# Optimization experiments

Hardware: AMD Instinct MI355X
Metric: run time of the kernel (lower is better)

Reference implementation:

```python
import jax, jax.numpy as jnp
import numpy as np

NUM_NODES = 50000
NUM_EDGES = 800000
NUM_GRAPHS = 64
EMBED = 128
HIDDEN = 128
LAYERS = 3
CLUSTERS = 16
OUT_DIM = 128
MAX_DEG = 64
EPS = 1e-5


def setup_inputs() -> dict:
    key = jax.random.key(0)
    ks = jax.random.split(key, 16)
    deg_idx = jax.random.randint(ks[0], (NUM_NODES,), 0, MAX_DEG + 1)
    edge_index = jax.random.randint(ks[1], (2, NUM_EDGES), 0, NUM_NODES)
    batch = jnp.sort(jax.random.randint(ks[2], (NUM_NODES,), 0, NUM_GRAPHS))
    s = 0.05
    emb = jax.random.normal(ks[3], (MAX_DEG + 1, EMBED), jnp.float32) * s
    Wl = jax.random.normal(ks[4], (LAYERS, HIDDEN, HIDDEN), jnp.float32) * s
    bl = jnp.zeros((LAYERS, HIDDEN), jnp.float32)
    Wr = jax.random.normal(ks[5], (LAYERS, HIDDEN, HIDDEN), jnp.float32) * s
    gamma = jnp.ones((LAYERS, HIDDEN), jnp.float32)
    beta = jnp.zeros((LAYERS, HIDDEN), jnp.float32)
    attn_W = jax.random.normal(ks[6], (HIDDEN, CLUSTERS), jnp.float32) * s
    attn_b = jnp.zeros((CLUSTERS,), jnp.float32)
    out_W = jax.random.normal(ks[7], (HIDDEN, OUT_DIM), jnp.float32) * s
    out_b = jnp.zeros((OUT_DIM,), jnp.float32)
    return {"emb": emb, "Wl": Wl, "bl": bl, "Wr": Wr, "gamma": gamma,
            "beta": beta, "attn_W": attn_W, "attn_b": attn_b,
            "out_W": out_W, "out_b": out_b, "deg_idx": deg_idx,
            "edge_index": edge_index, "batch": batch}


def reference(emb, Wl, bl, Wr, gamma, beta, attn_W, attn_b, out_W, out_b,
              deg_idx, edge_index, batch):
    N = deg_idx.shape[0]
    src, dst = edge_index[0], edge_index[1]
    x = emb[deg_idx]  # [N, EMBED]
    for l in range(Wl.shape[0]):
        # SAGEConv (mean aggr): lin_l(mean_j x_j) + lin_r(x); lin_r has no bias
        msg_sum = jax.ops.segment_sum(x[src], dst, num_segments=N)
        cnt = jax.ops.segment_sum(jnp.ones((src.shape[0], 1), x.dtype), dst,
                                  num_segments=N)
        mean = msg_sum / jnp.maximum(cnt, 1.0)
        x = mean @ Wl[l] + bl[l] + x @ Wr[l]
        # BatchNorm1d (training-mode batch stats, biased variance)
        mu = x.mean(axis=0)
        var = jnp.mean((x - mu) ** 2, axis=0)
        x = (x - mu) * jax.lax.rsqrt(var + EPS) * gamma[l] + beta[l]
        x = jax.nn.relu(x)  # dropout is identity in eval
    scores = x @ attn_W + attn_b  # [N, C] (num_heads == 1 -> squeeze)
    # per-graph softmax over nodes (segment softmax along dim 0)
    smax = jax.ops.segment_max(scores, batch, num_segments=NUM_GRAPHS)
    e = jnp.exp(scores - smax[batch])
    denom = jax.ops.segment_sum(e, batch, num_segments=NUM_GRAPHS)
    w = e / denom[batch]  # [N, C]
    # c_b = w_b^T @ x_b  -> segment-weighted sums: [B, C, H]
    clust = jax.ops.segment_sum(w[:, :, None] * x[:, None, :], batch,
                                num_segments=NUM_GRAPHS)
    return clust @ out_W + out_b  # [B, C, OUT_DIM]
```

## Files before the change

kernel.cpp:

```cpp
#include <hip/hip_runtime.h>

typedef unsigned short u16;
typedef unsigned int   u32;

#define H    128
#define C    16
#define ODIM 128

typedef short bf16x8 __attribute__((ext_vector_type(8)));
typedef float f32x4  __attribute__((ext_vector_type(4)));
typedef float f32x2v __attribute__((ext_vector_type(2)));

#define WSP 272
#define NP  256

__device__ __forceinline__ float bf2f(u32 v){
  union { u32 i; float f; } t; t.i = v << 16; return t.f;
}
__device__ __forceinline__ u16 f2bf(float f){
  u32 u = __float_as_uint(f);
  u32 r = u + 0x7fffu + ((u >> 16) & 1u);
  return (u16)(r >> 16);
}
__device__ __forceinline__ u32 pack2(float a, float b){
  return (u32)f2bf(a) | ((u32)f2bf(b) << 16);
}
__device__ __forceinline__ u32 pack_fp8x4(float a, float b, float c, float d){
  int p = __builtin_amdgcn_cvt_pk_fp8_f32(a, b, 0, false);
  p     = __builtin_amdgcn_cvt_pk_fp8_f32(c, d, p, true);
  return (u32)p;
}

__global__ __launch_bounds__(256) void k_setup(const float* __restrict__ emb,
    const int* __restrict__ deg, u16* __restrict__ xb, u32* __restrict__ xq,
    const int* __restrict__ batch, int* __restrict__ gs,
    const float* __restrict__ Wl, const float* __restrict__ Wr,
    u16* __restrict__ Wt, const int* __restrict__ ei,
    int* __restrict__ blkhist, int N, int B, int NB, int E, int chunk,
    int g0, int g1, int g2){
  __shared__ __align__(16) char smem[4608];
  int bid = blockIdx.x, tid = threadIdx.x;
  if (bid < g0){
    int i = bid*256 + tid;
    if (i < N*32){
      int n = i >> 5, q = i & 31;
      int d = deg[n];
      float4 v = ((const float4*)(emb + (size_t)d*H))[q];
      uint2 o; o.x = pack2(v.x, v.y); o.y = pack2(v.z, v.w);
      ((uint2*)(xb + (size_t)n*H))[q] = o;
      xq[i] = pack_fp8x4(v.x, v.y, v.z, v.w);
    }
  } else if (bid < g1){
    int n = (bid - g0)*256 + tid;
    if (n < N){
      int b = batch[n];
      if (n == 0){ for (int g = 0; g <= b; g++) gs[g] = 0; }
      else {
        int pb = batch[n-1];
        for (int g = pb+1; g <= b; g++) gs[g] = n;
      }
      if (n == N-1){ for (int g = b+1; g <= B; g++) gs[g] = N; }
    }
  } else if (bid < g2){
    u16 (*T)[18] = (u16(*)[18])smem;
    int b = bid - g1;
    int strip = b & 7, half = (b >> 3) & 1, l = b >> 4;
    const float* M = (half ? Wr : Wl) + (size_t)l*H*H;
    int k0 = strip * 16;
    #pragma unroll
    for (int j = 0; j < 8; j++){
      int u = tid + j*256;
      int kk = u >> 7, h = u & 127;
      T[h][kk] = f2bf(M[(size_t)(k0 + kk)*H + h]);
    }
    __syncthreads();
    #pragma unroll
    for (int j = 0; j < 8; j++){
      int u = tid + j*256;
      int h = u >> 4, k16 = u & 15;
      Wt[((size_t)(l*H + h))*256 + half*128 + k0 + k16] = T[h][k16];
    }
  } else {
    int* hist = (int*)smem;
    int blk = bid - g2;
    for (int b = tid; b < NB; b += 256) hist[b] = 0;
    __syncthreads();
    int start = blk*chunk, end = min(E, start + chunk);
    for (int e = start + tid; e < end; e += 256)
      atomicAdd(&hist[ei[E + e] >> 7], 1);
    __syncthreads();
    for (int b = tid; b < NB; b += 256) blkhist[b*NP + blk] = hist[b];
  }
}

__global__ __launch_bounds__(256) void k_scanA(const int* __restrict__ in,
    int* __restrict__ out, int* __restrict__ bsum, int n){
  __shared__ int wsum[4];
  int tid = threadIdx.x;
  int base = blockIdx.x*1024 + tid*4;
  int v0 = (base+0 < n) ? in[base+0] : 0;
  int v1 = (base+1 < n) ? in[base+1] : 0;
  int v2 = (base+2 < n) ? in[base+2] : 0;
  int v3 = (base+3 < n) ? in[base+3] : 0;
  int tsum = v0+v1+v2+v3;
  int lane = tid & 63, w = tid >> 6;
  int incl = tsum;
  for (int d = 1; d < 64; d <<= 1){
    int t = __shfl_up(incl, d, 64);
    if (lane >= d) incl += t;
  }
  if (lane == 63) wsum[w] = incl;
  __syncthreads();
  int woff = 0;
  for (int i = 0; i < w; i++) woff += wsum[i];
  int excl = woff + incl - tsum;
  if (base+0 < n) out[base+0] = excl;
  if (base+1 < n) out[base+1] = excl + v0;
  if (base+2 < n) out[base+2] = excl + v0 + v1;
  if (base+3 < n) out[base+3] = excl + v0 + v1 + v2;
  if (tid == 255) bsum[blockIdx.x] = woff + incl;
}

__global__ __launch_bounds__(256) void k_scanB(const int* __restrict__ bsum,
    int* __restrict__ boff, int nb){
  __shared__ int ws[4];
  int tid = threadIdx.x;
  int v = (tid < nb) ? bsum[tid] : 0;
  int lane = tid & 63, w = tid >> 6;
  int incl = v;
  for (int d = 1; d < 64; d <<= 1){
    int t = __shfl_up(incl, d, 64);
    if (lane >= d) incl += t;
  }
  if (lane == 63) ws[w] = incl;
  __syncthreads();
  int woff = 0;
  for (int i = 0; i < w; i++) woff += ws[i];
  boff[tid] = woff + incl - v;
}

__global__ __launch_bounds__(256) void k_place(const int* __restrict__ ei,
    const int* __restrict__ bases, const int* __restrict__ boff,
    int2* __restrict__ pairs, int NB, int E, int chunk){
  __shared__ int cursor[400];
  int blk = blockIdx.x, tid = threadIdx.x;
  for (int b = tid; b < NB; b += 256){
    int i = b*NP + blk;
    cursor[b] = bases[i] + boff[i >> 10];
  }
  __syncthreads();
  int start = blk*chunk, end = min(E, start + chunk);
  for (int e = start + tid; e < end; e += 256){
    int s = ei[e], d = ei[E + e];
    int pos = atomicAdd(&cursor[d >> 7], 1);
    pairs[pos] = make_int2(s, d);
  }
}

__global__ __launch_bounds__(256) void k_cnt_place(const int2* __restrict__ pairs,
    const int* __restrict__ bases, const int* __restrict__ boff,
    int* __restrict__ rowptr, int* __restrict__ col, int NB, int N, int E){
  int b = blockIdx.x, tid = threadIdx.x;
  int i0 = b*NP;
  int bstart = bases[i0] + boff[i0 >> 10];
  int bend = E;
  if (b+1 < NB){ int i1 = (b+1)*NP; bend = bases[i1] + boff[i1 >> 10]; }
  __shared__ int cnt[128], sc[128], rank[128];
  if (tid < 128) cnt[tid] = 0;
  __syncthreads();
  for (int e = bstart + tid; e < bend; e += 256)
    atomicAdd(&cnt[pairs[e].y & 127], 1);
  __syncthreads();
  if (tid < 128) sc[tid] = cnt[tid];
  for (int d = 1; d < 128; d <<= 1){
    int v = 0;
    __syncthreads();
    if (tid < 128 && tid >= d) v = sc[tid - d];
    __syncthreads();
    if (tid < 128) sc[tid] += v;
  }
  __syncthreads();
  if (tid < 128){
    int excl = sc[tid] - cnt[tid];
    rank[tid] = bstart + excl;
    int node = b*128 + tid;
    if (node < N) rowptr[node] = bstart + excl;
  }
  if (b == NB-1 && tid == 0) rowptr[N] = E;
  __syncthreads();
  for (int e = bstart + tid; e < bend; e += 256){
    int2 p = pairs[e];
    int pos = atomicAdd(&rank[p.y & 127], 1);
    col[pos] = p.x;
  }
}

__device__ __forceinline__ void dec16v(f32x2v* a, uint4 v){
  a[0] += __builtin_amdgcn_cvt_pk_f32_fp8((int)v.x, false);
  a[1] += __builtin_amdgcn_cvt_pk_f32_fp8((int)v.x, true );
  a[2] += __builtin_amdgcn_cvt_pk_f32_fp8((int)v.y, false);
  a[3] += __builtin_amdgcn_cvt_pk_f32_fp8((int)v.y, true );
  a[4] += __builtin_amdgcn_cvt_pk_f32_fp8((int)v.z, false);
  a[5] += __builtin_amdgcn_cvt_pk_f32_fp8((int)v.z, true );
  a[6] += __builtin_amdgcn_cvt_pk_f32_fp8((int)v.w, false);
  a[7] += __builtin_amdgcn_cvt_pk_f32_fp8((int)v.w, true );
}

__global__ __launch_bounds__(256) void k_agg(const u32* __restrict__ xq,
    const int* __restrict__ rowptr, const int* __restrict__ col,
    u16* __restrict__ meanb, int N){
  int wid  = (blockIdx.x*256 + threadIdx.x) >> 6;
  int lane = threadIdx.x & 63;
  if (wid >= N) return;
  int r0 = rowptr[wid], r1 = rowptr[wid+1];
  int grp = lane >> 3, fl = lane & 7;
  const u32* xf = xq + fl*4;
  f32x2v a[8];
  #pragma unroll
  for (int j = 0; j < 8; j++) a[j] = (f32x2v){0.f, 0.f};
  int e = r0 + grp;
  for (; e + 8 < r1; e += 16){
    uint4 v = *(const uint4*)(xf + (size_t)col[e]*32);
    uint4 u = *(const uint4*)(xf + (size_t)col[e+8]*32);
    dec16v(a, v);
    dec16v(a, u);
  }
  if (e < r1){
    uint4 v = *(const uint4*)(xf + (size_t)col[e]*32);
    dec16v(a, v);
  }
  #pragma unroll
  for (int j = 0; j < 8; j++){
    a[j].x += __shfl_xor(a[j].x, 8, 64);  a[j].y += __shfl_xor(a[j].y, 8, 64);
    a[j].x += __shfl_xor(a[j].x, 16, 64); a[j].y += __shfl_xor(a[j].y, 16, 64);
    a[j].x += __shfl_xor(a[j].x, 32, 64); a[j].y += __shfl_xor(a[j].y, 32, 64);
  }
  if (grp == 0){
    float invc = 1.0f / (float)max(r1 - r0, 1);
    uint4 o0, o1;
    o0.x = pack2(a[0].x*invc, a[0].y*invc);
    o0.y = pack2(a[1].x*invc, a[1].y*invc);
    o0.z = pack2(a[2].x*invc, a[2].y*invc);
    o0.w = pack2(a[3].x*invc, a[3].y*invc);
    o1.x = pack2(a[4].x*invc, a[4].y*invc);
    o1.y = pack2(a[5].x*invc, a[5].y*invc);
    o1.z = pack2(a[6].x*invc, a[6].y*invc);
    o1.w = pack2(a[7].x*invc, a[7].y*invc);
    u16* mp = meanb + (size_t)wid*H + fl*16;
    *(uint4*)mp       = o0;
    *(uint4*)(mp + 8) = o1;
  }
}

__global__ __launch_bounds__(256) void k_linear(const u16* __restrict__ meanb,
    const u16* __restrict__ xb, const u16* __restrict__ Wt,
    const float* __restrict__ bl, u16* __restrict__ x2b,
    float* __restrict__ pstats, int N){
  __shared__ u16 Ws[128][WSP];
  __shared__ float Sh[128], Qh[128];
  int tid = threadIdx.x;
  if (tid < 128){ Sh[tid] = 0.f; Qh[tid] = 0.f; }
  int lane = tid & 63, w = tid >> 6;
  int mlane = lane & 15, quad = lane >> 4;
  int node = blockIdx.x*64 + w*16 + mlane;
  const u16* arow_m = meanb + (size_t)node*H + quad*8;
  const u16* arow_x = xb   + (size_t)node*H + quad*8;
  bf16x8 af[8];
  #pragma unroll
  for (int kk = 0; kk < 4; kk++){
    af[kk]     = *(const bf16x8*)(arow_m + kk*32);
    af[kk + 4] = *(const bf16x8*)(arow_x + kk*32);
  }
  #pragma unroll
  for (int j = 0; j < 16; j++){
    int u = tid + j*256;
    int row = u >> 5, seg = u & 31;
    uint4 v = ((const uint4*)(Wt + (size_t)row*256))[seg];
    *(uint4*)&Ws[row][seg*8] = v;
  }
  __syncthreads();
  f32x4 acc[8];
  #pragma unroll
  for (int t = 0; t < 8; t++) acc[t] = (f32x4){0.f, 0.f, 0.f, 0.f};
  #pragma unroll
  for (int kk = 0; kk < 8; kk++){
    #pragma unroll
    for (int t = 0; t < 8; t++){
      bf16x8 b = *(const bf16x8*)&Ws[t*16 + mlane][kk*32 + quad*8];
      acc[t] = __builtin_amdgcn_mfma_f32_16x16x32_bf16(af[kk], b, acc[t], 0, 0, 0);
    }
  }
  #pragma unroll
  for (int t = 0; t < 8; t++){
    int h = t*16 + mlane;
    float bv = bl[h];
    float s = 0.f, q = 0.f;
    #pragma unroll
    for (int r = 0; r < 4; r++){
      int nd = blockIdx.x*64 + w*16 + quad*4 + r;
      if (nd < N){
        float v = acc[t][r] + bv;
        x2b[(size_t)nd*H + h] = f2bf(v);
        s += v; q = fmaf(v, v, q);
      }
    }
    s += __shfl_xor(s, 16, 64); s += __shfl_xor(s, 32, 64);
    q += __shfl_xor(q, 16, 64); q += __shfl_xor(q, 32, 64);
    if (quad == 0){
      atomicAdd(&Sh[h], s);
      atomicAdd(&Qh[h], q);
    }
  }
  __syncthreads();
  {
    float v = (tid < 128) ? Sh[tid] : Qh[tid - 128];
    pstats[(size_t)blockIdx.x*256 + tid] = v;
  }
}

__global__ __launch_bounds__(256) void k_statred(const float* __restrict__ pstats,
    float* __restrict__ stats, int nblk){
  __shared__ float red[4];
  int c = blockIdx.x, tid = threadIdx.x;
  float s = 0.f;
  for (int b = tid; b < nblk; b += 256)
    s += pstats[(size_t)b*256 + c];
  s += __shfl_xor(s, 1, 64);  s += __shfl_xor(s, 2, 64);
  s += __shfl_xor(s, 4, 64);  s += __shfl_xor(s, 8, 64);
  s += __shfl_xor(s, 16, 64); s += __shfl_xor(s, 32, 64);
  if ((tid & 63) == 0) red[tid >> 6] = s;
  __syncthreads();
  if (tid == 0) stats[c] = red[0] + red[1] + red[2] + red[3];
}

__global__ __launch_bounds__(256) void k_bnrelu(const u16* __restrict__ x2b,
    const float* __restrict__ stats, const float* __restrict__ gamma,
    const float* __restrict__ beta, u16* __restrict__ xb, u32* __restrict__ xq,
    int N, float invN,
    const float* __restrict__ attn_W, const float* __restrict__ attn_b,
    float* __restrict__ escore, int do_scores){
  __shared__ float xs[8][132];
  __shared__ float aw[H*C];
  __shared__ float ab[C];
  int tid = threadIdx.x;
  int i = blockIdx.x*256 + tid;
  bool active = (i < N*32);
  int h = (tid & 31) * 4;
  float r[4] = {0.f, 0.f, 0.f, 0.f};
  if (active){
    uint2 o2 = ((const uint2*)x2b)[i];
    float vv[4] = {bf2f(o2.x & 0xffff), bf2f(o2.x >> 16),
                   bf2f(o2.y & 0xffff), bf2f(o2.y >> 16)};
    #pragma unroll
    for (int j = 0; j < 4; j++){
      float mu  = stats[h+j] * invN;
      float var = fmaf(-mu, mu, stats[H + h + j] * invN);
      float sc  = rsqrtf(var + 1e-5f) * gamma[h+j];
      float bi  = beta[h+j];
      r[j] = fmaxf(fmaf(vv[j] - mu, sc, bi), 0.0f);
    }
    uint2 o; o.x = pack2(r[0], r[1]); o.y = pack2(r[2], r[3]);
    ((uint2*)xb)[i] = o;
    xq[i] = pack_fp8x4(r[0], r[1], r[2], r[3]);
  }
  if (do_scores){
    #pragma unroll
    for (int j = 0; j < 8; j++) aw[tid + j*256] = attn_W[tid + j*256];
    if (tid < C) ab[tid] = attn_b[tid];
    int ln = tid >> 5;
    if (active){
      xs[ln][h+0]=r[0]; xs[ln][h+1]=r[1]; xs[ln][h+2]=r[2]; xs[ln][h+3]=r[3];
    }
    __syncthreads();
    if (tid < 128){
      int n2 = tid >> 4, c = tid & 15;
      int node = blockIdx.x*8 + n2;
      if (node < N){
        float acc = ab[c];
        #pragma unroll 4
        for (int k = 0; k < H; k++)
          acc = fmaf(xs[n2][k], aw[k*C + c], acc);
        escore[(size_t)node*C + c] = __expf(acc);
      }
    }
  }
}

__global__ __launch_bounds__(256) void k_clust(const u16* __restrict__ xb,
    const float* __restrict__ escore, const int* __restrict__ gs,
    float* __restrict__ partial){
  int g = blockIdx.x >> 4, b = blockIdx.x & 15;
  int h = threadIdx.x & 127, cg = threadIdx.x >> 7;
  int a = gs[g], e2 = gs[g+1];
  float acc[8] = {0,0,0,0,0,0,0,0};
  for (int n = a + b; n < e2; n += 16){
    float xv = bf2f(xb[(size_t)n*H + h]);
    const float4* ep = (const float4*)(escore + (size_t)n*C) + cg*2;
    float4 e0 = ep[0], e1 = ep[1];
    acc[0] = fmaf(e0.x, xv, acc[0]);
    acc[1] = fmaf(e0.y, xv, acc[1]);
    acc[2] = fmaf(e0.z, xv, acc[2]);
    acc[3] = fmaf(e0.w, xv, acc[3]);
    acc[4] = fmaf(e1.x, xv, acc[4]);
    acc[5] = fmaf(e1.y, xv, acc[5]);
    acc[6] = fmaf(e1.z, xv, acc[6]);
    acc[7] = fmaf(e1.w, xv, acc[7]);
  }
  int c0 = cg*8;
  float* dst = partial + (((size_t)(g*16 + b))*C)*H + h;
  #pragma unroll
  for (int r = 0; r < 8; r++)
    dst[(size_t)(c0 + r)*H] = acc[r];
}

__global__ __launch_bounds__(256) void k_out(const float* __restrict__ partial,
    const float* __restrict__ escore, const int* __restrict__ gs,
    const float* __restrict__ out_W, const float* __restrict__ out_b,
    float* __restrict__ out){
  __shared__ float cs[2][128];
  __shared__ float dsum[4];
  int tid = threadIdx.x;
  int r = tid >> 7, h = tid & 127;
  int row = blockIdx.x*2 + r;
  int g = row >> 4, c = row & 15;
  int a = gs[g], b2 = gs[g+1];
  float s = 0.f;
  for (int n = a + h; n < b2; n += 128) s += escore[(size_t)n*C + c];
  s += __shfl_xor(s, 1, 64);  s += __shfl_xor(s, 2, 64);
  s += __shfl_xor(s, 4, 64);  s += __shfl_xor(s, 8, 64);
  s += __shfl_xor(s, 16, 64); s += __shfl_xor(s, 32, 64);
  if ((tid & 63) == 0) dsum[tid >> 6] = s;
  float p = 0.f;
  for (int b = 0; b < 16; b++)
    p += partial[(((size_t)(g*16 + b))*C + c)*H + h];
  cs[r][h] = p;
  __syncthreads();
  float gden = dsum[r*2] + dsum[r*2 + 1];
  float inv = gden > 0.f ? 1.0f / gden : 0.f;
  float acc = 0.f;
  for (int hh = 0; hh < H; hh++)
    acc = fmaf(cs[r][hh], out_W[hh*ODIM + h], acc);
  out[(size_t)row*ODIM + h] = fmaf(acc, inv, out_b[h]);
}

extern "C" void kernel_launch(void* const* d_in, const int* in_sizes, int n_in,
                              void* d_out, int out_size, void* d_ws, size_t ws_size,
                              hipStream_t stream){
  const float* emb    = (const float*)d_in[0];
  const float* Wl     = (const float*)d_in[1];
  const float* bl     = (const float*)d_in[2];
  const float* Wr     = (const float*)d_in[3];
  const float* gamma  = (const float*)d_in[4];
  const float* beta   = (const float*)d_in[5];
  const float* attn_W = (const float*)d_in[6];
  const float* attn_b = (const float*)d_in[7];
  const float* out_W  = (const float*)d_in[8];
  const float* out_b  = (const float*)d_in[9];
  const int* deg    = (const int*)d_in[10];
  const int* ei     = (const int*)d_in[11];
  const int* batch  = (const int*)d_in[12];
  float* out = (float*)d_out;

  const int N = in_sizes[10];
  const int E = in_sizes[11] / 2;
  const int L = in_sizes[1] / (H*H);
  const int B = out_size / (C*ODIM);
  const int NB = (N + 127) >> 7;
  const int nbh = NB * NP;
  const int chunk = (E + NP - 1) / NP;
  const int nblkL = (N + 63) / 64;

  size_t off = 0;
  auto alloc = [&](size_t bytes) -> void* {
    void* p = (char*)d_ws + off;
    off += (bytes + 255) & ~(size_t)255;
    return p;
  };
  u16*   xb     = (u16*)  alloc((size_t)N*H*2);
  u32*   xq     = (u32*)  alloc((size_t)N*H);
  u16*   meanb  = (u16*)  alloc((size_t)N*H*2);
  u16*   x2b    = (u16*)  alloc((size_t)N*H*2);
  int2*  pairs  = (int2*) alloc((size_t)E*8);
  float* partial= (float*)alloc((size_t)B*16*C*H*4);
  u16*   Wt     = (u16*)  alloc((size_t)L*H*256*2);
  float* escore = (float*)alloc((size_t)N*C*4);
  int*   col    = (int*)  alloc((size_t)E*4);
  int*   rowptr = (int*)  alloc((size_t)(N+1)*4);
  int*   blkhist= (int*)  alloc((size_t)nbh*4);
  int*   bases  = (int*)  alloc((size_t)nbh*4);
  int*   bsum   = (int*)  alloc(256*4);
  int*   boff   = (int*)  alloc(256*4);
  int*   gs     = (int*)  alloc((size_t)(B+1)*4);
  float* stats  = (float*)alloc((size_t)L*2*H*4);
  float* pstats = (float*)alloc((size_t)nblkL*256*4);

  int g0 = (N*32 + 255)/256;
  int g1 = g0 + (N + 255)/256;
  int g2 = g1 + L*16;
  int gT = g2 + NP;
  hipLaunchKernelGGL(k_setup, dim3(gT), dim3(256), 0, stream,
                     emb, deg, xb, xq, batch, gs, Wl, Wr, Wt, ei, blkhist,
                     N, B, NB, E, chunk, g0, g1, g2);
  int nblkS = (nbh + 1023) / 1024;
  hipLaunchKernelGGL(k_scanA, dim3(nblkS), dim3(256), 0, stream, blkhist, bases, bsum, nbh);
  hipLaunchKernelGGL(k_scanB, dim3(1),     dim3(256), 0, stream, bsum, boff, nblkS);
  hipLaunchKernelGGL(k_place, dim3(NP), dim3(256), 0, stream,
                     ei, bases, boff, pairs, NB, E, chunk);
  hipLaunchKernelGGL(k_cnt_place, dim3(NB), dim3(256), 0, stream,
                     pairs, bases, boff, rowptr, col, NB, N, E);

  float invN = 1.0f / (float)N;
  for (int l = 0; l < L; l++){
    hipLaunchKernelGGL(k_agg,    dim3((N+3)/4),  dim3(256), 0, stream, xq, rowptr, col, meanb, N);
    hipLaunchKernelGGL(k_linear, dim3(nblkL),    dim3(256), 0, stream,
                       meanb, xb, Wt + (size_t)l*H*256, bl + (size_t)l*H, x2b,
                       pstats, N);
    hipLaunchKernelGGL(k_statred,dim3(256),      dim3(256), 0, stream, pstats, stats + l*2*H, nblkL);
    hipLaunchKernelGGL(k_bnrelu, dim3((N*32+255)/256), dim3(256), 0, stream,
                       x2b, stats + l*2*H, gamma + (size_t)l*H, beta + (size_t)l*H,
                       xb, xq, N, invN, attn_W, attn_b, escore, (l == L-1) ? 1 : 0);
  }
  hipLaunchKernelGGL(k_clust, dim3(B*16),  dim3(256), 0, stream, xb, escore, gs, partial);
  hipLaunchKernelGGL(k_out,   dim3(B*C/2), dim3(256), 0, stream,
                     partial, escore, gs, out_W, out_b, out);
}
```

Before: 335.5 us.

## Remove scanB and statred launches via inline scan and sharded atomic stats

The single-block bsum scan is now recomputed inside each block of k_place and k_cnt_place, so the separate k_scanB launch goes away. The per-block BatchNorm partial stats are now accumulated with float atomics into 16 shards that are zeroed in k_setup, and each k_bnrelu block sums those shards itself, which drops the k_statred launch every layer. This cuts four kernel launches and their serial gaps. In exchange it adds redundant scan work per block, atomic contention on the shards, and run-to-run nondeterminism in the stats sums.

```diff
diff --git a/kernel.cpp b/kernel.cpp
--- a/kernel.cpp
+++ b/kernel.cpp
@@ -13,6 +13,7 @@
 
 #define WSP 272
 #define NP  256
+#define NSH 16
 
 __device__ __forceinline__ float bf2f(u32 v){
   union { u32 i; float f; } t; t.i = v << 16; return t.f;
@@ -36,12 +37,15 @@
     const int* __restrict__ batch, int* __restrict__ gs,
     const float* __restrict__ Wl, const float* __restrict__ Wr,
     u16* __restrict__ Wt, const int* __restrict__ ei,
-    int* __restrict__ blkhist, int N, int B, int NB, int E, int chunk,
-    int g0, int g1, int g2){
+    int* __restrict__ blkhist, float* __restrict__ statsh,
+    int N, int B, int NB, int E, int chunk,
+    int gz, int g0, int g1, int g2){
   __shared__ __align__(16) char smem[4608];
   int bid = blockIdx.x, tid = threadIdx.x;
-  if (bid < g0){
-    int i = bid*256 + tid;
+  if (bid < gz){
+    statsh[bid*256 + tid] = 0.f;
+  } else if (bid < g0){
+    int i = (bid - gz)*256 + tid;
     if (i < N*32){
       int n = i >> 5, q = i & 31;
       int d = deg[n];
@@ -121,10 +125,9 @@
   if (tid == 255) bsum[blockIdx.x] = woff + incl;
 }
 
-__global__ __launch_bounds__(256) void k_scanB(const int* __restrict__ bsum,
-    int* __restrict__ boff, int nb){
-  __shared__ int ws[4];
-  int tid = threadIdx.x;
+__device__ __forceinline__ void scan_bsum(const int* __restrict__ bsum,
+    int* bo, int nb, int tid){
+  __shared__ int ws2[4];
   int v = (tid < nb) ? bsum[tid] : 0;
   int lane = tid & 63, w = tid >> 6;
   int incl = v;
@@ -132,21 +135,24 @@
     int t = __shfl_up(incl, d, 64);
     if (lane >= d) incl += t;
   }
-  if (lane == 63) ws[w] = incl;
+  if (lane == 63) ws2[w] = incl;
   __syncthreads();
   int woff = 0;
-  for (int i = 0; i < w; i++) woff += ws[i];
-  boff[tid] = woff + incl - v;
+  for (int i = 0; i < w; i++) woff += ws2[i];
+  bo[tid] = woff + incl - v;
+  __syncthreads();
 }
 
 __global__ __launch_bounds__(256) void k_place(const int* __restrict__ ei,
-    const int* __restrict__ bases, const int* __restrict__ boff,
-    int2* __restrict__ pairs, int NB, int E, int chunk){
+    const int* __restrict__ bases, const int* __restrict__ bsum,
+    int2* __restrict__ pairs, int NB, int E, int chunk, int nbs){
   __shared__ int cursor[400];
+  __shared__ int bo[256];
   int blk = blockIdx.x, tid = threadIdx.x;
+  scan_bsum(bsum, bo, nbs, tid);
   for (int b = tid; b < NB; b += 256){
     int i = b*NP + blk;
-    cursor[b] = bases[i] + boff[i >> 10];
+    cursor[b] = bases[i] + bo[i >> 10];
   }
   __syncthreads();
   int start = blk*chunk, end = min(E, start + chunk);
@@ -158,13 +164,16 @@
 }
 
 __global__ __launch_bounds__(256) void k_cnt_place(const int2* __restrict__ pairs,
-    const int* __restrict__ bases, const int* __restrict__ boff,
-    int* __restrict__ rowptr, int* __restrict__ col, int NB, int N, int E){
+    const int* __restrict__ bases, const int* __restrict__ bsum,
+    int* __restrict__ rowptr, int* __restrict__ col,
+    int NB, int N, int E, int nbs){
   int b = blockIdx.x, tid = threadIdx.x;
+  __shared__ int bo[256];
+  scan_bsum(bsum, bo, nbs, tid);
   int i0 = b*NP;
-  int bstart = bases[i0] + boff[i0 >> 10];
+  int bstart = bases[i0] + bo[i0 >> 10];
   int bend = E;
-  if (b+1 < NB){ int i1 = (b+1)*NP; bend = bases[i1] + boff[i1 >> 10]; }
+  if (b+1 < NB){ int i1 = (b+1)*NP; bend = bases[i1] + bo[i1 >> 10]; }
   __shared__ int cnt[128], sc[128], rank[128];
   if (tid < 128) cnt[tid] = 0;
   __syncthreads();
@@ -255,7 +264,7 @@
 __global__ __launch_bounds__(256) void k_linear(const u16* __restrict__ meanb,
     const u16* __restrict__ xb, const u16* __restrict__ Wt,
     const float* __restrict__ bl, u16* __restrict__ x2b,
-    float* __restrict__ pstats, int N){
+    float* __restrict__ statsh_l, int N){
   __shared__ u16 Ws[128][WSP];
   __shared__ float Sh[128], Qh[128];
   int tid = threadIdx.x;
@@ -314,35 +323,28 @@
   __syncthreads();
   {
     float v = (tid < 128) ? Sh[tid] : Qh[tid - 128];
-    pstats[(size_t)blockIdx.x*256 + tid] = v;
-  }
-}
-
-__global__ __launch_bounds__(256) void k_statred(const float* __restrict__ pstats,
-    float* __restrict__ stats, int nblk){
-  __shared__ float red[4];
-  int c = blockIdx.x, tid = threadIdx.x;
-  float s = 0.f;
-  for (int b = tid; b < nblk; b += 256)
-    s += pstats[(size_t)b*256 + c];
-  s += __shfl_xor(s, 1, 64);  s += __shfl_xor(s, 2, 64);
-  s += __shfl_xor(s, 4, 64);  s += __shfl_xor(s, 8, 64);
-  s += __shfl_xor(s, 16, 64); s += __shfl_xor(s, 32, 64);
-  if ((tid & 63) == 0) red[tid >> 6] = s;
-  __syncthreads();
-  if (tid == 0) stats[c] = red[0] + red[1] + red[2] + red[3];
+    atomicAdd(&statsh_l[(blockIdx.x & (NSH-1))*256 + tid], v);
+  }
 }
 
 __global__ __launch_bounds__(256) void k_bnrelu(const u16* __restrict__ x2b,
-    const float* __restrict__ stats, const float* __restrict__ gamma,
+    const float* __restrict__ statsh_l, const float* __restrict__ gamma,
     const float* __restrict__ beta, u16* __restrict__ xb, u32* __restrict__ xq,
     int N, float invN,
     const float* __restrict__ attn_W, const float* __restrict__ attn_b,
     float* __restrict__ escore, int do_scores){
+  __shared__ float st[256];
   __shared__ float xs[8][132];
   __shared__ float aw[H*C];
   __shared__ float ab[C];
   int tid = threadIdx.x;
+  {
+    float sacc = 0.f;
+    #pragma unroll
+    for (int s2 = 0; s2 < NSH; s2++) sacc += statsh_l[s2*256 + tid];
+    st[tid] = sacc;
+  }
+  __syncthreads();
   int i = blockIdx.x*256 + tid;
   bool active = (i < N*32);
   int h = (tid & 31) * 4;
@@ -353,8 +355,8 @@
                    bf2f(o2.y & 0xffff), bf2f(o2.y >> 16)};
     #pragma unroll
     for (int j = 0; j < 4; j++){
-      float mu  = stats[h+j] * invN;
-      float var = fmaf(-mu, mu, stats[H + h + j] * invN);
+      float mu  = st[h+j] * invN;
+      float var = fmaf(-mu, mu, st[H + h + j] * invN);
       float sc  = rsqrtf(var + 1e-5f) * gamma[h+j];
       float bi  = beta[h+j];
       r[j] = fmaxf(fmaf(vv[j] - mu, sc, bi), 0.0f);
@@ -489,35 +491,33 @@
   int*   blkhist= (int*)  alloc((size_t)nbh*4);
   int*   bases  = (int*)  alloc((size_t)nbh*4);
   int*   bsum   = (int*)  alloc(256*4);
-  int*   boff   = (int*)  alloc(256*4);
   int*   gs     = (int*)  alloc((size_t)(B+1)*4);
-  float* stats  = (float*)alloc((size_t)L*2*H*4);
-  float* pstats = (float*)alloc((size_t)nblkL*256*4);
-
-  int g0 = (N*32 + 255)/256;
+  float* statsh = (float*)alloc((size_t)L*NSH*256*4);
+
+  int gz = L*NSH;
+  int g0 = gz + (N*32 + 255)/256;
   int g1 = g0 + (N + 255)/256;
   int g2 = g1 + L*16;
   int gT = g2 + NP;
   hipLaunchKernelGGL(k_setup, dim3(gT), dim3(256), 0, stream,
                      emb, deg, xb, xq, batch, gs, Wl, Wr, Wt, ei, blkhist,
-                     N, B, NB, E, chunk, g0, g1, g2);
+                     statsh, N, B, NB, E, chunk, gz, g0, g1, g2);
   int nblkS = (nbh + 1023) / 1024;
   hipLaunchKernelGGL(k_scanA, dim3(nblkS), dim3(256), 0, stream, blkhist, bases, bsum, nbh);
-  hipLaunchKernelGGL(k_scanB, dim3(1),     dim3(256), 0, stream, bsum, boff, nblkS);
   hipLaunchKernelGGL(k_place, dim3(NP), dim3(256), 0, stream,
-                     ei, bases, boff, pairs, NB, E, chunk);
+                     ei, bases, bsum, pairs, NB, E, chunk, nblkS);
   hipLaunchKernelGGL(k_cnt_place, dim3(NB), dim3(256), 0, stream,
-                     pairs, bases, boff, rowptr, col, NB, N, E);
+                     pairs, bases, bsum, rowptr, col, NB, N, E, nblkS);
 
   float invN = 1.0f / (float)N;
   for (int l = 0; l < L; l++){
+    float* sh_l = statsh + (size_t)l*NSH*256;
     hipLaunchKernelGGL(k_agg,    dim3((N+3)/4),  dim3(256), 0, stream, xq, rowptr, col, meanb, N);
     hipLaunchKernelGGL(k_linear, dim3(nblkL),    dim3(256), 0, stream,
                        meanb, xb, Wt + (size_t)l*H*256, bl + (size_t)l*H, x2b,
-                       pstats, N);
-    hipLaunchKernelGGL(k_statred,dim3(256),      dim3(256), 0, stream, pstats, stats + l*2*H, nblkL);
+                       sh_l, N);
     hipLaunchKernelGGL(k_bnrelu, dim3((N*32+255)/256), dim3(256), 0, stream,
-                       x2b, stats + l*2*H, gamma + (size_t)l*H, beta + (size_t)l*H,
+                       x2b, sh_l, gamma + (size_t)l*H, beta + (size_t)l*H,
                        xb, xq, N, invN, attn_W, attn_b, escore, (l == L-1) ? 1 : 0);
   }
   hipLaunchKernelGGL(k_clust, dim3(B*16),  dim3(256), 0, stream, xb, escore, gs, partial);
```

After: 333.6 us. Within noise of the previous version (-0.6%).
